# Kernel optimization log

Hardware: AMD Instinct MI355X
Metric: run time of the kernel (lower is better)

The kernel has to match this reference:

```python
import jax, jax.numpy as jnp
import numpy as np
from jax import lax

B_, N_, DIM, HID, DST, NT, IR, DTR, HH, WW = 16, 4096, 192, 384, 16, 17, 128, 24, 64, 64


def _selective_scan(u, delta, A, Bs, Cs, D, delta_bias):
    # u, delta: (B, Din, L); A: (Din, N); Bs, Cs: (B, N, L); D, delta_bias: (Din,)
    delta = jax.nn.softplus(delta + delta_bias[None, :, None])
    dT = jnp.moveaxis(delta, 2, 0)   # (L, B, Din)
    uT = jnp.moveaxis(u, 2, 0)       # (L, B, Din)
    BT = jnp.moveaxis(Bs, 2, 0)      # (L, B, N)
    CT = jnp.moveaxis(Cs, 2, 0)      # (L, B, N)
    Bsz, Din, L = u.shape
    Nst = A.shape[1]
    h0 = jnp.zeros((Bsz, Din, Nst), u.dtype)

    def step(h, inp):
        d_l, u_l, b_l, c_l = inp
        da = jnp.exp(d_l[:, :, None] * A[None])              # (B, Din, N)
        h = da * h + (d_l * u_l)[:, :, None] * b_l[:, None, :]
        y = jnp.einsum('bdn,bn->bd', h, c_l)
        return h, y

    _, ys = lax.scan(step, h0, (dT, uT, BT, CT))
    y = jnp.moveaxis(ys, 0, 2)                               # (B, Din, L)
    return y + u * D[None, :, None]


def _assm_forward(x, token_weight, gumbel_noise, embB, route_w1, route_b1, route_w2,
                  route_b2, inproj_w, inproj_b, cpe_w, cpe_b, x_proj_w, dt_w, dt_b,
                  A_logs, Ds, norm_g, norm_b, outproj_w, outproj_b, H, W, gather_type):
    B, n, C = x.shape
    hidden = inproj_w.shape[0]
    dst = token_weight.shape[1]
    dtr = dt_w.shape[1]

    # routing + gumbel-softmax (hard, straight-through)
    full_emb = embB @ token_weight                           # (NT, d_state)
    hmid = jax.nn.gelu(x @ route_w1.T + route_b1)
    logits = jax.nn.log_softmax(hmid @ route_w2.T + route_b2, axis=-1)
    y_soft = jax.nn.softmax(logits + gumbel_noise, axis=-1)
    idx = jnp.argmax(y_soft, axis=-1)                        # (B, n)
    y_hard = jax.nn.one_hot(idx, logits.shape[-1], dtype=y_soft.dtype)
    cls_policy = y_hard + y_soft - lax.stop_gradient(y_soft)
    prompt = cls_policy @ full_emb                           # (B, n, d_state)

    det = lax.stop_gradient(idx)
    # (gather_type 3/5 keypoint-group remap omitted: gather_type == 1 here)
    sort_idx = jnp.argsort(det, axis=-1)                     # (B, n)
    inv_idx = jnp.argsort(sort_idx, axis=-1)                 # index_reverse

    # in_proj (1x1 conv == pointwise linear) then depthwise CPE gate
    xi = x @ inproj_w.T + inproj_b                           # (B, n, hidden)
    xg = xi.reshape(B, H, W, hidden).transpose(0, 3, 1, 2)   # NCHW
    cpe = lax.conv_general_dilated(xg, cpe_w, (1, 1), 'SAME',
                                   feature_group_count=hidden,
                                   dimension_numbers=('NCHW', 'OIHW', 'NCHW'))
    cpe = cpe + cpe_b[None, :, None, None]
    xg = xg * jax.nn.sigmoid(cpe)
    xflat = xg.reshape(B, hidden, n).transpose(0, 2, 1)      # (B, n, hidden)

    sem_x = jnp.take_along_axis(xflat, sort_idx[:, :, None], axis=1)

    # Selective_Scan core
    xs = sem_x.transpose(0, 2, 1)                            # (B, Din, L)
    x_dbl = jnp.einsum('bdl,cd->bcl', xs, x_proj_w)          # (B, dtr+2N, L)
    dts, Bs, Cs = jnp.split(x_dbl, [dtr, dtr + dst], axis=1)
    dts = jnp.einsum('brl,dr->bdl', dts, dt_w)
    if gather_type != 0:
        Cs = Cs + prompt.transpose(0, 2, 1)
    A = -jnp.exp(A_logs)
    y = _selective_scan(xs, dts, A, Bs, Cs, Ds, dt_b)        # (B, Din, L)
    y = y.transpose(0, 2, 1)                                 # (B, L, hidden)

    mu = jnp.mean(y, axis=-1, keepdims=True)
    var = jnp.mean(jnp.square(y - mu), axis=-1, keepdims=True)
    yn = (y - mu) / jnp.sqrt(var + 1e-5) * norm_g + norm_b
    out = yn @ outproj_w.T + outproj_b                       # (B, n, dim)
    out = jnp.take_along_axis(out, inv_idx[:, :, None], axis=1)
    return out


def setup_inputs() -> dict:
    key = jax.random.key(0)
    ks = jax.random.split(key, 16)

    def rn(k, sh, s=0.02):
        return jax.random.normal(k, sh, dtype=jnp.float32) * s

    u = jax.random.uniform(ks[0], (B_, N_, NT), jnp.float32, 1e-6, 1.0 - 1e-6)
    gumbel = -jnp.log(-jnp.log(u))

    # faithful dt bias init (inverse-softplus of log-uniform dt)
    rng = np.random.default_rng(0)
    dt = np.exp(rng.uniform(size=HID) * (np.log(0.1) - np.log(0.001)) + np.log(0.001))
    dt = np.clip(dt, 1e-4, None)
    inv_dt = dt + np.log(-np.expm1(-dt))

    A_logs = jnp.log(jnp.tile(jnp.arange(1, DST + 1, dtype=jnp.float32), (HID, 1)))

    return {
        'x': jax.random.normal(ks[1], (B_, N_, DIM), jnp.float32),
        'token_weight': rn(ks[2], (IR, DST), 0.1),
        'gumbel_noise': gumbel,
        'embB': jax.random.uniform(ks[3], (NT, IR), jnp.float32, -1.0 / NT, 1.0 / NT),
        'route_w1': rn(ks[4], (DIM // 3, DIM)),
        'route_b1': jnp.zeros((DIM // 3,), jnp.float32),
        'route_w2': rn(ks[5], (NT, DIM // 3)),
        'route_b2': jnp.zeros((NT,), jnp.float32),
        'inproj_w': rn(ks[6], (HID, DIM)),
        'inproj_b': jnp.zeros((HID,), jnp.float32),
        'cpe_w': rn(ks[7], (HID, 1, 3, 3), 0.1),
        'cpe_b': jnp.zeros((HID,), jnp.float32),
        'x_proj_w': rn(ks[8], (DTR + 2 * DST, HID)),
        'dt_w': jax.random.uniform(ks[9], (HID, DTR), jnp.float32, -DTR ** -0.5, DTR ** -0.5),
        'dt_b': jnp.asarray(inv_dt, jnp.float32),
        'A_logs': A_logs,
        'Ds': jnp.ones((HID,), jnp.float32),
        'norm_g': jnp.ones((HID,), jnp.float32),
        'norm_b': jnp.zeros((HID,), jnp.float32),
        'outproj_w': rn(ks[10], (DIM, HID)),
        'outproj_b': jnp.zeros((DIM,), jnp.float32),
        'H': HH,
        'W': WW,
        'gather_type': 1,
    }


def reference(x, token_weight, gumbel_noise, embB, route_w1, route_b1, route_w2,
              route_b2, inproj_w, inproj_b, cpe_w, cpe_b, x_proj_w, dt_w, dt_b,
              A_logs, Ds, norm_g, norm_b, outproj_w, outproj_b, H, W, gather_type):
    return _assm_forward(x, token_weight, gumbel_noise, embB, route_w1, route_b1,
                         route_w2, route_b2, inproj_w, inproj_b, cpe_w, cpe_b,
                         x_proj_w, dt_w, dt_b, A_logs, Ds, norm_g, norm_b,
                         outproj_w, outproj_b, H, W, gather_type)
```

## Files before the change

kernel.cpp:

```cpp
#include <hip/hip_runtime.h>
#include <math.h>

#define NB 16
#define NL 4096
#define ND 192
#define NH 384
#define NS 16
#define NTK 17
#define NIR 128
#define NR 24
#define NHH 64
#define NWW 64
#define NCHUNKS 32
#define CHUNKLEN 128
#define NTOK (NB*NL)

typedef __attribute__((ext_vector_type(8))) short short8;
typedef __attribute__((ext_vector_type(4))) float floatx4;

__device__ __forceinline__ float gelu_tanh(float x){
  return 0.5f*x*(1.0f + tanhf(0.7978845608028654f*(x + 0.044715f*x*x*x)));
}
__device__ __forceinline__ float softplus_f(float x){
  return (x > 20.0f) ? x : log1pf(expf(x));
}
__device__ __forceinline__ short f2bf(float f){
  unsigned u = __float_as_uint(f);
  unsigned r = (u + 0x7fffu + ((u >> 16) & 1u)) >> 16;
  return (short)r;
}

union Pack8 { uint4 v; short s[8]; };

__global__ void k_emb(const float* __restrict__ embB, const float* __restrict__ tw,
                      float* __restrict__ fe){
  for (int o = threadIdx.x; o < NTK*NS; o += 256){
    int t = o / NS, s = o % NS;
    float acc = 0.f;
    for (int i = 0; i < NIR; ++i) acc += embB[t*NIR+i]*tw[i*NS+s];
    fe[o] = acc;
  }
}

__global__ void k_cvtw(const float* __restrict__ inw, const float* __restrict__ ow,
                       const float* __restrict__ xpw, const float* __restrict__ dtw,
                       short* __restrict__ inwb, short* __restrict__ owb,
                       short* __restrict__ xpwb, short* __restrict__ dtwb){
  int i = blockIdx.x*256 + threadIdx.x;
  int stride = gridDim.x*256;
  for (int p = i; p < NH*ND; p += stride) inwb[p] = f2bf(inw[p]);
  for (int p = i; p < ND*NH; p += stride) owb[p] = f2bf(ow[p]);
  for (int p = i; p < 56*NH; p += stride) xpwb[p] = f2bf(xpw[p]);
  for (int p = i; p < NH*32; p += stride){
    int r = p >> 5, c = p & 31;
    dtwb[p] = (c < NR) ? f2bf(dtw[r*NR + c]) : (short)0;
  }
}

template<int EPI>
__global__ __launch_bounds__(256) void k_gemm(const float* __restrict__ A, int lda,
    const float* __restrict__ W, int ldw, const float* __restrict__ bias,
    float* __restrict__ C, int ldc, int N, int K){
  __shared__ float As[16][68];
  __shared__ float Ws[16][68];
  int tid = threadIdx.x;
  int m0 = blockIdx.x*64, n0 = blockIdx.y*64;
  int tx = tid & 15, ty = tid >> 4;
  int srow = tid >> 2, skseg = (tid & 3)*4;
  float acc[4][4] = {};
  for (int k0 = 0; k0 < K; k0 += 16){
    {
      const float* ap = A + (size_t)(m0+srow)*lda + k0 + skseg;
      float4 v = *(const float4*)ap;
      As[skseg+0][srow]=v.x; As[skseg+1][srow]=v.y;
      As[skseg+2][srow]=v.z; As[skseg+3][srow]=v.w;
    }
    {
      float4 v = {0.f,0.f,0.f,0.f};
      if (n0 + srow < N) v = *(const float4*)(W + (size_t)(n0+srow)*ldw + k0 + skseg);
      Ws[skseg+0][srow]=v.x; Ws[skseg+1][srow]=v.y;
      Ws[skseg+2][srow]=v.z; Ws[skseg+3][srow]=v.w;
    }
    __syncthreads();
    #pragma unroll
    for (int kk = 0; kk < 16; ++kk){
      float4 av = *(const float4*)&As[kk][ty*4];
      float4 wv = *(const float4*)&Ws[kk][tx*4];
      acc[0][0] += av.x*wv.x; acc[0][1] += av.x*wv.y;
      acc[0][2] += av.x*wv.z; acc[0][3] += av.x*wv.w;
      acc[1][0] += av.y*wv.x; acc[1][1] += av.y*wv.y;
      acc[1][2] += av.y*wv.z; acc[1][3] += av.y*wv.w;
      acc[2][0] += av.z*wv.x; acc[2][1] += av.z*wv.y;
      acc[2][2] += av.z*wv.z; acc[2][3] += av.z*wv.w;
      acc[3][0] += av.w*wv.x; acc[3][1] += av.w*wv.y;
      acc[3][2] += av.w*wv.z; acc[3][3] += av.w*wv.w;
    }
    __syncthreads();
  }
  #pragma unroll
  for (int i = 0; i < 4; ++i){
    int m = m0 + ty*4 + i;
    #pragma unroll
    for (int j = 0; j < 4; ++j){
      int n = n0 + tx*4 + j;
      if (n < N){
        float v = acc[i][j] + (bias ? bias[n] : 0.f);
        if (EPI==1) v = gelu_tanh(v);
        C[(size_t)m*ldc + n] = v;
      }
    }
  }
}

template<int EPI, int AF32>
__global__ __launch_bounds__(256) void k_mfma(const void* __restrict__ Aptr, int lda,
    const short* __restrict__ Wbf, int ldw, const float* __restrict__ bias,
    float* __restrict__ C, int ldc, int N, int K, const int* __restrict__ remap){
  __shared__ short As[128*40];
  __shared__ short Bs[64*40];
  int tid = threadIdx.x;
  int m0 = blockIdx.x*128, n0 = blockIdx.y*64;
  int w = tid >> 6, lane = tid & 63;
  int lq = lane >> 4, lr = lane & 15;
  floatx4 acc[2][4];
  #pragma unroll
  for (int i = 0; i < 2; ++i)
    #pragma unroll
    for (int j = 0; j < 4; ++j) acc[i][j] = (floatx4){0.f,0.f,0.f,0.f};
  int ar = tid >> 1, aq = (tid & 1)*2;
  int br = tid >> 2, bq = tid & 3;
  for (int k0 = 0; k0 < K; k0 += 32){
    Pack8 sa0, sa1;
    if (AF32){
      const float* ap = (const float*)Aptr + (size_t)(m0+ar)*lda + k0 + aq*8;
      float4 f0 = *(const float4*)(ap);
      float4 f1 = *(const float4*)(ap+4);
      float4 f2 = *(const float4*)(ap+8);
      float4 f3 = *(const float4*)(ap+12);
      sa0.s[0]=f2bf(f0.x); sa0.s[1]=f2bf(f0.y); sa0.s[2]=f2bf(f0.z); sa0.s[3]=f2bf(f0.w);
      sa0.s[4]=f2bf(f1.x); sa0.s[5]=f2bf(f1.y); sa0.s[6]=f2bf(f1.z); sa0.s[7]=f2bf(f1.w);
      sa1.s[0]=f2bf(f2.x); sa1.s[1]=f2bf(f2.y); sa1.s[2]=f2bf(f2.z); sa1.s[3]=f2bf(f2.w);
      sa1.s[4]=f2bf(f3.x); sa1.s[5]=f2bf(f3.y); sa1.s[6]=f2bf(f3.z); sa1.s[7]=f2bf(f3.w);
    } else {
      const short* ap = (const short*)Aptr + (size_t)(m0+ar)*lda + k0 + aq*8;
      sa0.v = *(const uint4*)ap;
      sa1.v = *(const uint4*)(ap + 8);
    }
    uint4 bv = {0u,0u,0u,0u};
    if (n0 + br < N) bv = *(const uint4*)(Wbf + (size_t)(n0+br)*ldw + k0 + bq*8);
    __syncthreads();
    *(uint4*)&As[ar*40 + aq*8]     = sa0.v;
    *(uint4*)&As[ar*40 + aq*8 + 8] = sa1.v;
    *(uint4*)&Bs[br*40 + bq*8]     = bv;
    __syncthreads();
    short8 a0 = *(const short8*)&As[(w*32      + lr)*40 + lq*8];
    short8 a1 = *(const short8*)&As[(w*32 + 16 + lr)*40 + lq*8];
    short8 b0 = *(const short8*)&Bs[(     lr)*40 + lq*8];
    short8 b1 = *(const short8*)&Bs[(16 + lr)*40 + lq*8];
    short8 b2 = *(const short8*)&Bs[(32 + lr)*40 + lq*8];
    short8 b3 = *(const short8*)&Bs[(48 + lr)*40 + lq*8];
    acc[0][0] = __builtin_amdgcn_mfma_f32_16x16x32_bf16(a0, b0, acc[0][0], 0,0,0);
    acc[0][1] = __builtin_amdgcn_mfma_f32_16x16x32_bf16(a0, b1, acc[0][1], 0,0,0);
    acc[0][2] = __builtin_amdgcn_mfma_f32_16x16x32_bf16(a0, b2, acc[0][2], 0,0,0);
    acc[0][3] = __builtin_amdgcn_mfma_f32_16x16x32_bf16(a0, b3, acc[0][3], 0,0,0);
    acc[1][0] = __builtin_amdgcn_mfma_f32_16x16x32_bf16(a1, b0, acc[1][0], 0,0,0);
    acc[1][1] = __builtin_amdgcn_mfma_f32_16x16x32_bf16(a1, b1, acc[1][1], 0,0,0);
    acc[1][2] = __builtin_amdgcn_mfma_f32_16x16x32_bf16(a1, b2, acc[1][2], 0,0,0);
    acc[1][3] = __builtin_amdgcn_mfma_f32_16x16x32_bf16(a1, b3, acc[1][3], 0,0,0);
  }
  #pragma unroll
  for (int mt = 0; mt < 2; ++mt){
    #pragma unroll
    for (int r = 0; r < 4; ++r){
      int m = m0 + w*32 + mt*16 + lq*4 + r;
      int orow = (EPI==3) ? remap[m] : m;
      #pragma unroll
      for (int nt = 0; nt < 4; ++nt){
        int n = n0 + nt*16 + lr;
        if (n < N){
          float v = acc[mt][nt][r] + (bias ? bias[n] : 0.f);
          if (EPI==2) v = softplus_f(v);
          C[(size_t)orow*ldc + n] = v;
        }
      }
    }
  }
}

__global__ __launch_bounds__(256) void k_argmax(const float* __restrict__ hmid,
    const float* __restrict__ w2, const float* __restrict__ b2,
    const float* __restrict__ gumbel, int* __restrict__ idx){
  int g = blockIdx.x*256 + threadIdx.x;
  float hm[64];
  const float4* hp = (const float4*)(hmid + (size_t)g*64);
  #pragma unroll
  for (int i = 0; i < 16; ++i){
    float4 v = hp[i];
    hm[i*4+0]=v.x; hm[i*4+1]=v.y; hm[i*4+2]=v.z; hm[i*4+3]=v.w;
  }
  float best = -INFINITY; int bi = 0;
  for (int c = 0; c < NTK; ++c){
    float s = b2[c] + gumbel[(size_t)g*NTK + c];
    #pragma unroll
    for (int j = 0; j < 64; ++j) s += hm[j]*w2[c*64+j];
    if (s > best){ best = s; bi = c; }
  }
  idx[g] = bi;
}

__global__ __launch_bounds__(256) void k_sort(const int* __restrict__ idx,
    int* __restrict__ rmap, int* __restrict__ inv){
  int b = blockIdx.x, t = threadIdx.x;
  __shared__ int hist[NTK][256];
  __shared__ int tot[NTK];
  __shared__ int keybase[NTK];
  int keys[16];
  const int* ip = idx + b*NL + t*16;
  #pragma unroll
  for (int i = 0; i < 16; ++i) keys[i] = ip[i];
  #pragma unroll
  for (int k = 0; k < NTK; ++k){
    int c = 0;
    #pragma unroll
    for (int i = 0; i < 16; ++i) c += (keys[i]==k) ? 1 : 0;
    hist[k][t] = c;
  }
  __syncthreads();
  if (t < NTK){
    int run = 0;
    for (int j = 0; j < 256; ++j){ int v = hist[t][j]; hist[t][j] = run; run += v; }
    tot[t] = run;
  }
  __syncthreads();
  if (t == 0){
    int base = 0;
    for (int k = 0; k < NTK; ++k){ keybase[k] = base; base += tot[k]; }
  }
  __syncthreads();
  #pragma unroll
  for (int i = 0; i < 16; ++i){
    int k = keys[i];
    int cb = 0;
    #pragma unroll
    for (int j = 0; j < 16; ++j) cb += (j < i && keys[j]==k) ? 1 : 0;
    int pos = keybase[k] + hist[k][t] + cb;
    rmap[b*NL + pos] = b*NL + t*16 + i;
    inv[b*NL + t*16 + i] = pos;
  }
}

__global__ __launch_bounds__(256) void k_cpe(const float* __restrict__ xi,
    const float* __restrict__ cw, const float* __restrict__ cb,
    const int* __restrict__ inv, float* __restrict__ us){
  int bl = blockIdx.x;
  int cg = bl & 3;
  int xt = (bl>>2) & 7;
  int yt = (bl>>5) & 7;
  int b  = bl >> 8;
  __shared__ float tile[10*10*96];
  int c0 = cg*96;
  for (int p = threadIdx.x; p < 10*10*96; p += 256){
    int c = p % 96; int xx = (p/96) % 10; int yy = p/960;
    int gy = yt*8 + yy - 1, gx = xt*8 + xx - 1;
    float v = 0.f;
    if (gy >= 0 && gy < NHH && gx >= 0 && gx < NWW)
      v = xi[((size_t)(b*NL + gy*NWW + gx))*NH + c0 + c];
    tile[p] = v;
  }
  __syncthreads();
  for (int p = threadIdx.x; p < 8*8*96; p += 256){
    int c = p % 96; int xx = (p/96) % 8; int yy = p/768;
    int ch = c0 + c;
    float acc = cb[ch];
    #pragma unroll
    for (int dy = 0; dy < 3; ++dy)
      #pragma unroll
      for (int dx = 0; dx < 3; ++dx)
        acc += tile[((yy+dy)*10 + (xx+dx))*96 + c] * cw[ch*9 + dy*3 + dx];
    float center = tile[((yy+1)*10 + (xx+1))*96 + c];
    float gate = 1.f/(1.f + expf(-acc));
    int l = (yt*8+yy)*NWW + xt*8+xx;
    int pos = inv[b*NL + l];
    us[((size_t)(b*NL + pos))*NH + ch] = center*gate;
  }
}

__global__ __launch_bounds__(256) void k_bc(const float* __restrict__ dbl,
    const int* __restrict__ idx, const float* __restrict__ fe,
    const int* __restrict__ gt, float* __restrict__ Bsb, float* __restrict__ Csb,
    short* __restrict__ dtsb){
  int g = blockIdx.x*256 + threadIdx.x;
  const float* dr = dbl + (size_t)g*56;
  int id = idx[g];
  int gather = gt[0];
  #pragma unroll
  for (int n = 0; n < NR; ++n) dtsb[(size_t)g*32 + n] = f2bf(dr[n]);
  #pragma unroll
  for (int n = NR; n < 32; ++n) dtsb[(size_t)g*32 + n] = 0;
  #pragma unroll
  for (int n = 0; n < NS; ++n){
    Bsb[(size_t)g*NS + n] = dr[24+n];
    float c = dr[40+n];
    if (gather != 0) c += fe[id*NS + n];
    Csb[(size_t)g*NS + n] = c;
  }
}

__device__ __forceinline__ void decay16(bool pw, float dlt, const float* An, float* a){
  if (pw){
    float r = __expf(dlt*An[0]);
    a[0] = r;
    #pragma unroll
    for (int n = 1; n < NS; ++n) a[n] = a[n-1]*r;
  } else {
    #pragma unroll
    for (int n = 0; n < NS; ++n) a[n] = __expf(dlt*An[n]);
  }
}
__device__ __forceinline__ bool pwcheck(const float* An){
  bool pw = true;
  #pragma unroll
  for (int n = 1; n < NS; ++n)
    pw = pw && (fabsf(An[n] - (n+1)*An[0]) <= 1e-4f*fabsf(An[n]));
  return pw;
}

__global__ __launch_bounds__(384) void k_scan1(const float* __restrict__ delta,
    const float* __restrict__ us, const float* __restrict__ Bsb,
    const float* __restrict__ A_logs, float* __restrict__ Aprod, float* __restrict__ Boff){
  int bc = blockIdx.x;
  int c = bc & (NCHUNKS-1);
  int b = bc >> 5;
  int d = threadIdx.x;
  __shared__ float Bsh[CHUNKLEN*NS];
  int base = b*NL + c*CHUNKLEN;
  for (int p = d; p < CHUNKLEN*NS; p += 384) Bsh[p] = Bsb[(size_t)base*NS + p];
  float An[NS];
  #pragma unroll
  for (int n = 0; n < NS; ++n) An[n] = -expf(A_logs[d*NS + n]);
  bool pw = pwcheck(An);
  float h[NS], ap[NS];
  #pragma unroll
  for (int n = 0; n < NS; ++n){ h[n]=0.f; ap[n]=1.f; }
  __syncthreads();
  for (int s = 0; s < CHUNKLEN; ++s){
    size_t gi = (size_t)(base + s)*NH + d;
    float dlt = delta[gi];
    float uv = us[gi];
    float du = dlt*uv;
    float a[NS];
    decay16(pw, dlt, An, a);
    #pragma unroll
    for (int n = 0; n < NS; ++n){
      ap[n] *= a[n];
      h[n] = a[n]*h[n] + du*Bsh[s*NS+n];
    }
  }
  size_t o = ((size_t)bc*NH + d)*NS;
  #pragma unroll
  for (int n = 0; n < NS; ++n){ Aprod[o+n]=ap[n]; Boff[o+n]=h[n]; }
}

__global__ __launch_bounds__(256) void k_scan2(const float* __restrict__ Aprod,
    float* __restrict__ Boff){
  int i = blockIdx.x*256 + threadIdx.x;
  int dn = i % (NH*NS);
  int b = i / (NH*NS);
  float h = 0.f;
  for (int c = 0; c < NCHUNKS; ++c){
    size_t o = ((size_t)(b*NCHUNKS + c)*NH*NS) + dn;
    float a = Aprod[o];
    float bo = Boff[o];
    Boff[o] = h;
    h = a*h + bo;
  }
}

__global__ __launch_bounds__(384) void k_scan3(const float* __restrict__ delta,
    const float* __restrict__ Bsb, const float* __restrict__ Csb,
    const float* __restrict__ A_logs, const float* __restrict__ Ds,
    const float* __restrict__ hinit, float* __restrict__ us){
  int bc = blockIdx.x;
  int c = bc & (NCHUNKS-1);
  int b = bc >> 5;
  int d = threadIdx.x;
  __shared__ float Bsh[CHUNKLEN*NS];
  __shared__ float Csh[CHUNKLEN*NS];
  int base = b*NL + c*CHUNKLEN;
  for (int p = d; p < CHUNKLEN*NS; p += 384){
    Bsh[p] = Bsb[(size_t)base*NS + p];
    Csh[p] = Csb[(size_t)base*NS + p];
  }
  float An[NS];
  #pragma unroll
  for (int n = 0; n < NS; ++n) An[n] = -expf(A_logs[d*NS + n]);
  bool pw = pwcheck(An);
  float h[NS];
  size_t ho = ((size_t)bc*NH + d)*NS;
  #pragma unroll
  for (int n = 0; n < NS; ++n) h[n] = hinit[ho + n];
  float Dd = Ds[d];
  __syncthreads();
  for (int s = 0; s < CHUNKLEN; ++s){
    size_t gi = (size_t)(base + s)*NH + d;
    float dlt = delta[gi];
    float uv = us[gi];
    float du = dlt*uv;
    float a[NS];
    decay16(pw, dlt, An, a);
    float y = 0.f;
    #pragma unroll
    for (int n = 0; n < NS; ++n){
      h[n] = a[n]*h[n] + du*Bsh[s*NS+n];
      y += h[n]*Csh[s*NS+n];
    }
    us[gi] = y + uv*Dd;
  }
}

__global__ __launch_bounds__(256) void k_ln(float* __restrict__ y,
    const float* __restrict__ gw, const float* __restrict__ gb){
  int g = blockIdx.x*4 + (threadIdx.x >> 6);
  int lane = threadIdx.x & 63;
  size_t ro = (size_t)g*NH;
  float v[6];
  #pragma unroll
  for (int i = 0; i < 6; ++i) v[i] = y[ro + i*64 + lane];
  float s = 0.f;
  #pragma unroll
  for (int i = 0; i < 6; ++i) s += v[i];
  #pragma unroll
  for (int off = 32; off > 0; off >>= 1) s += __shfl_xor(s, off);
  float mean = s * (1.f/NH);
  float vs = 0.f;
  #pragma unroll
  for (int i = 0; i < 6; ++i){ float d = v[i]-mean; vs += d*d; }
  #pragma unroll
  for (int off = 32; off > 0; off >>= 1) vs += __shfl_xor(vs, off);
  float rstd = rsqrtf(vs*(1.f/NH) + 1e-5f);
  #pragma unroll
  for (int i = 0; i < 6; ++i){
    int col = i*64 + lane;
    y[ro+col] = (v[i]-mean)*rstd*gw[col] + gb[col];
  }
}

extern "C" void kernel_launch(void* const* d_in, const int* in_sizes, int n_in,
                              void* d_out, int out_size, void* d_ws, size_t ws_size,
                              hipStream_t stream){
  const float* x      = (const float*)d_in[0];
  const float* tw     = (const float*)d_in[1];
  const float* gumbel = (const float*)d_in[2];
  const float* embB   = (const float*)d_in[3];
  const float* rw1    = (const float*)d_in[4];
  const float* rb1    = (const float*)d_in[5];
  const float* rw2    = (const float*)d_in[6];
  const float* rb2    = (const float*)d_in[7];
  const float* inw    = (const float*)d_in[8];
  const float* inb    = (const float*)d_in[9];
  const float* cw     = (const float*)d_in[10];
  const float* cb     = (const float*)d_in[11];
  const float* xpw    = (const float*)d_in[12];
  const float* dtw    = (const float*)d_in[13];
  const float* dtb    = (const float*)d_in[14];
  const float* A_logs = (const float*)d_in[15];
  const float* Ds     = (const float*)d_in[16];
  const float* ng     = (const float*)d_in[17];
  const float* nbv    = (const float*)d_in[18];
  const float* ow     = (const float*)d_in[19];
  const float* ob     = (const float*)d_in[20];
  const int*   gt     = (const int*)d_in[23];
  float* out = (float*)d_out;

  float* ws = (float*)d_ws;
  size_t o = 0;
  float* fe   = ws + o; o += 512;
  int* idx    = (int*)(ws + o); o += NTOK;
  int* rmap   = (int*)(ws + o); o += NTOK;
  int* inv    = (int*)(ws + o); o += NTOK;
  float* hmid = ws + o; o += (size_t)NTOK*64;
  float* xi   = ws + o; o += (size_t)NTOK*NH;
  float* us   = ws + o; o += (size_t)NTOK*NH;
  float* Bsb  = ws + o; o += (size_t)NTOK*NS;
  float* Csb  = ws + o; o += (size_t)NTOK*NS;
  float* Apr  = ws + o; o += (size_t)NB*NCHUNKS*NH*NS;
  float* Bof  = ws + o; o += (size_t)NB*NCHUNKS*NH*NS;
  short* inwb = (short*)(ws + o); o += (NH*ND)/2;
  short* owb  = (short*)(ws + o); o += (ND*NH)/2;
  short* xpwb = (short*)(ws + o); o += (56*NH)/2 + 32;
  short* dtwb = (short*)(ws + o); o += (NH*32)/2;
  float* dbl = hmid;
  float* delta = xi;
  short* dtsb = (short*)Apr;

  k_emb<<<1,256,0,stream>>>(embB, tw, fe);
  k_cvtw<<<64,256,0,stream>>>(inw, ow, xpw, dtw, inwb, owb, xpwb, dtwb);
  k_gemm<1><<<dim3(NTOK/64,1),256,0,stream>>>(x, ND, rw1, ND, rb1, hmid, 64, 64, ND);
  k_argmax<<<NTOK/256,256,0,stream>>>(hmid, rw2, rb2, gumbel, idx);
  k_sort<<<NB,256,0,stream>>>(idx, rmap, inv);
  k_mfma<0,1><<<dim3(NTOK/128,6),256,0,stream>>>(x, ND, inwb, ND, inb, xi, NH, NH, ND, nullptr);
  k_cpe<<<NB*64*4,256,0,stream>>>(xi, cw, cb, inv, us);
  k_mfma<0,1><<<dim3(NTOK/128,1),256,0,stream>>>(us, NH, xpwb, NH, nullptr, dbl, 56, 56, NH, nullptr);
  k_bc<<<NTOK/256,256,0,stream>>>(dbl, idx, fe, gt, Bsb, Csb, dtsb);
  k_mfma<2,0><<<dim3(NTOK/128,6),256,0,stream>>>(dtsb, 32, dtwb, 32, dtb, delta, NH, NH, 32, nullptr);
  k_scan1<<<NB*NCHUNKS,384,0,stream>>>(delta, us, Bsb, A_logs, Apr, Bof);
  k_scan2<<<(NB*NH*NS)/256,256,0,stream>>>(Apr, Bof);
  k_scan3<<<NB*NCHUNKS,384,0,stream>>>(delta, Bsb, Csb, A_logs, Ds, Bof, us);
  k_ln<<<NTOK/4,256,0,stream>>>(us, ng, nbv);
  k_mfma<3,1><<<dim3(NTOK/128,3),256,0,stream>>>(us, NH, owb, NH, ob, out, ND, ND, NH, rmap);
}
```

Baseline: 785.1 us.

## Fuse LayerNorm apply into out_proj GEMM and cheapen scan decay products

LayerNorm now only computes per-row mean and rstd, and the normalization with gamma/beta is applied while the out-projection GEMM loads its A tile. This avoids a full write and re-read of the 384-wide activation. In scan1 the running product of decays is replaced by a single decay evaluated on the summed delta, and the power-series decay uses a shallower multiply tree. Both scan loops are unrolled by 2. The trade-offs are that the normalization is recomputed for each of the three N-tiles of the GEMM, and the workspace buffers idx/inv are reused for the statistics.

```diff
diff --git a/kernel.cpp b/kernel.cpp
--- a/kernel.cpp
+++ b/kernel.cpp
@@ -112,10 +112,12 @@
   }
 }
 
-template<int EPI, int AF32>
+template<int EPI, int AF32, int LNA>
 __global__ __launch_bounds__(256) void k_mfma(const void* __restrict__ Aptr, int lda,
     const short* __restrict__ Wbf, int ldw, const float* __restrict__ bias,
-    float* __restrict__ C, int ldc, int N, int K, const int* __restrict__ remap){
+    float* __restrict__ C, int ldc, int N, int K, const int* __restrict__ remap,
+    const float* __restrict__ lnm, const float* __restrict__ lnr,
+    const float* __restrict__ lng, const float* __restrict__ lnb){
   __shared__ short As[128*40];
   __shared__ short Bs[64*40];
   int tid = threadIdx.x;
@@ -129,18 +131,29 @@
     for (int j = 0; j < 4; ++j) acc[i][j] = (floatx4){0.f,0.f,0.f,0.f};
   int ar = tid >> 1, aq = (tid & 1)*2;
   int br = tid >> 2, bq = tid & 3;
+  float mr = 0.f, rr = 0.f;
+  if (LNA){ mr = lnm[m0+ar]; rr = lnr[m0+ar]; }
   for (int k0 = 0; k0 < K; k0 += 32){
     Pack8 sa0, sa1;
     if (AF32){
       const float* ap = (const float*)Aptr + (size_t)(m0+ar)*lda + k0 + aq*8;
+      float f[16];
       float4 f0 = *(const float4*)(ap);
       float4 f1 = *(const float4*)(ap+4);
       float4 f2 = *(const float4*)(ap+8);
       float4 f3 = *(const float4*)(ap+12);
-      sa0.s[0]=f2bf(f0.x); sa0.s[1]=f2bf(f0.y); sa0.s[2]=f2bf(f0.z); sa0.s[3]=f2bf(f0.w);
-      sa0.s[4]=f2bf(f1.x); sa0.s[5]=f2bf(f1.y); sa0.s[6]=f2bf(f1.z); sa0.s[7]=f2bf(f1.w);
-      sa1.s[0]=f2bf(f2.x); sa1.s[1]=f2bf(f2.y); sa1.s[2]=f2bf(f2.z); sa1.s[3]=f2bf(f2.w);
-      sa1.s[4]=f2bf(f3.x); sa1.s[5]=f2bf(f3.y); sa1.s[6]=f2bf(f3.z); sa1.s[7]=f2bf(f3.w);
+      f[0]=f0.x; f[1]=f0.y; f[2]=f0.z; f[3]=f0.w;
+      f[4]=f1.x; f[5]=f1.y; f[6]=f1.z; f[7]=f1.w;
+      f[8]=f2.x; f[9]=f2.y; f[10]=f2.z; f[11]=f2.w;
+      f[12]=f3.x; f[13]=f3.y; f[14]=f3.z; f[15]=f3.w;
+      if (LNA){
+        const float* gp = lng + k0 + aq*8;
+        const float* bp = lnb + k0 + aq*8;
+        #pragma unroll
+        for (int j = 0; j < 16; ++j) f[j] = (f[j]-mr)*rr*gp[j] + bp[j];
+      }
+      #pragma unroll
+      for (int j = 0; j < 8; ++j){ sa0.s[j] = f2bf(f[j]); sa1.s[j] = f2bf(f[8+j]); }
     } else {
       const short* ap = (const short*)Aptr + (size_t)(m0+ar)*lda + k0 + aq*8;
       sa0.v = *(const uint4*)ap;
@@ -308,10 +321,16 @@
 
 __device__ __forceinline__ void decay16(bool pw, float dlt, const float* An, float* a){
   if (pw){
-    float r = __expf(dlt*An[0]);
-    a[0] = r;
-    #pragma unroll
-    for (int n = 1; n < NS; ++n) a[n] = a[n-1]*r;
+    float r  = __expf(dlt*An[0]);
+    float r2 = r*r;
+    float r3 = r2*r;
+    float r4 = r2*r2;
+    float r8 = r4*r4;
+    float r12 = r8*r4;
+    a[0]=r;     a[1]=r2;     a[2]=r3;     a[3]=r4;
+    a[4]=r4*r;  a[5]=r4*r2;  a[6]=r4*r3;  a[7]=r8;
+    a[8]=r8*r;  a[9]=r8*r2;  a[10]=r8*r3; a[11]=r12;
+    a[12]=r12*r; a[13]=r12*r2; a[14]=r12*r3; a[15]=r8*r8;
   } else {
     #pragma unroll
     for (int n = 0; n < NS; ++n) a[n] = __expf(dlt*An[n]);
@@ -339,23 +358,25 @@
   #pragma unroll
   for (int n = 0; n < NS; ++n) An[n] = -expf(A_logs[d*NS + n]);
   bool pw = pwcheck(An);
-  float h[NS], ap[NS];
-  #pragma unroll
-  for (int n = 0; n < NS; ++n){ h[n]=0.f; ap[n]=1.f; }
+  float h[NS];
+  #pragma unroll
+  for (int n = 0; n < NS; ++n) h[n]=0.f;
+  float sd = 0.f;
   __syncthreads();
+  #pragma unroll 2
   for (int s = 0; s < CHUNKLEN; ++s){
     size_t gi = (size_t)(base + s)*NH + d;
     float dlt = delta[gi];
     float uv = us[gi];
     float du = dlt*uv;
+    sd += dlt;
     float a[NS];
     decay16(pw, dlt, An, a);
     #pragma unroll
-    for (int n = 0; n < NS; ++n){
-      ap[n] *= a[n];
-      h[n] = a[n]*h[n] + du*Bsh[s*NS+n];
-    }
-  }
+    for (int n = 0; n < NS; ++n) h[n] = a[n]*h[n] + du*Bsh[s*NS+n];
+  }
+  float ap[NS];
+  decay16(pw, sd, An, ap);
   size_t o = ((size_t)bc*NH + d)*NS;
   #pragma unroll
   for (int n = 0; n < NS; ++n){ Aprod[o+n]=ap[n]; Boff[o+n]=h[n]; }
@@ -401,6 +422,7 @@
   for (int n = 0; n < NS; ++n) h[n] = hinit[ho + n];
   float Dd = Ds[d];
   __syncthreads();
+  #pragma unroll 2
   for (int s = 0; s < CHUNKLEN; ++s){
     size_t gi = (size_t)(base + s)*NH + d;
     float dlt = delta[gi];
@@ -418,8 +440,8 @@
   }
 }
 
-__global__ __launch_bounds__(256) void k_ln(float* __restrict__ y,
-    const float* __restrict__ gw, const float* __restrict__ gb){
+__global__ __launch_bounds__(256) void k_lnstat(const float* __restrict__ y,
+    float* __restrict__ mean, float* __restrict__ rstd){
   int g = blockIdx.x*4 + (threadIdx.x >> 6);
   int lane = threadIdx.x & 63;
   size_t ro = (size_t)g*NH;
@@ -431,18 +453,14 @@
   for (int i = 0; i < 6; ++i) s += v[i];
   #pragma unroll
   for (int off = 32; off > 0; off >>= 1) s += __shfl_xor(s, off);
-  float mean = s * (1.f/NH);
+  float mu = s * (1.f/NH);
   float vs = 0.f;
   #pragma unroll
-  for (int i = 0; i < 6; ++i){ float d = v[i]-mean; vs += d*d; }
+  for (int i = 0; i < 6; ++i){ float d = v[i]-mu; vs += d*d; }
   #pragma unroll
   for (int off = 32; off > 0; off >>= 1) vs += __shfl_xor(vs, off);
-  float rstd = rsqrtf(vs*(1.f/NH) + 1e-5f);
-  #pragma unroll
-  for (int i = 0; i < 6; ++i){
-    int col = i*64 + lane;
-    y[ro+col] = (v[i]-mean)*rstd*gw[col] + gb[col];
-  }
+  float rs = rsqrtf(vs*(1.f/NH) + 1e-5f);
+  if (lane == 0){ mean[g] = mu; rstd[g] = rs; }
 }
 
 extern "C" void kernel_launch(void* const* d_in, const int* in_sizes, int n_in,
@@ -492,20 +510,26 @@
   float* dbl = hmid;
   float* delta = xi;
   short* dtsb = (short*)Apr;
+  float* lnmean = (float*)idx;
+  float* lnrstd = (float*)inv;
 
   k_emb<<<1,256,0,stream>>>(embB, tw, fe);
   k_cvtw<<<64,256,0,stream>>>(inw, ow, xpw, dtw, inwb, owb, xpwb, dtwb);
   k_gemm<1><<<dim3(NTOK/64,1),256,0,stream>>>(x, ND, rw1, ND, rb1, hmid, 64, 64, ND);
   k_argmax<<<NTOK/256,256,0,stream>>>(hmid, rw2, rb2, gumbel, idx);
   k_sort<<<NB,256,0,stream>>>(idx, rmap, inv);
-  k_mfma<0,1><<<dim3(NTOK/128,6),256,0,stream>>>(x, ND, inwb, ND, inb, xi, NH, NH, ND, nullptr);
+  k_mfma<0,1,0><<<dim3(NTOK/128,6),256,0,stream>>>(x, ND, inwb, ND, inb, xi, NH, NH, ND,
+      nullptr, nullptr, nullptr, nullptr, nullptr);
   k_cpe<<<NB*64*4,256,0,stream>>>(xi, cw, cb, inv, us);
-  k_mfma<0,1><<<dim3(NTOK/128,1),256,0,stream>>>(us, NH, xpwb, NH, nullptr, dbl, 56, 56, NH, nullptr);
+  k_mfma<0,1,0><<<dim3(NTOK/128,1),256,0,stream>>>(us, NH, xpwb, NH, nullptr, dbl, 56, 56, NH,
+      nullptr, nullptr, nullptr, nullptr, nullptr);
   k_bc<<<NTOK/256,256,0,stream>>>(dbl, idx, fe, gt, Bsb, Csb, dtsb);
-  k_mfma<2,0><<<dim3(NTOK/128,6),256,0,stream>>>(dtsb, 32, dtwb, 32, dtb, delta, NH, NH, 32, nullptr);
+  k_mfma<2,0,0><<<dim3(NTOK/128,6),256,0,stream>>>(dtsb, 32, dtwb, 32, dtb, delta, NH, NH, 32,
+      nullptr, nullptr, nullptr, nullptr, nullptr);
   k_scan1<<<NB*NCHUNKS,384,0,stream>>>(delta, us, Bsb, A_logs, Apr, Bof);
   k_scan2<<<(NB*NH*NS)/256,256,0,stream>>>(Apr, Bof);
   k_scan3<<<NB*NCHUNKS,384,0,stream>>>(delta, Bsb, Csb, A_logs, Ds, Bof, us);
-  k_ln<<<NTOK/4,256,0,stream>>>(us, ng, nbv);
-  k_mfma<3,1><<<dim3(NTOK/128,3),256,0,stream>>>(us, NH, owb, NH, ob, out, ND, ND, NH, rmap);
-}
+  k_lnstat<<<NTOK/4,256,0,stream>>>(us, lnmean, lnrstd);
+  k_mfma<3,1,1><<<dim3(NTOK/128,3),256,0,stream>>>(us, NH, owb, NH, ob, out, ND, ND, NH,
+      rmap, lnmean, lnrstd, ng, nbv);
+}
```

Result: faster. 761.9 us (-3.0%).
